# Kernel optimization log

Measured on AMD Instinct MI355X. Metric: run time of the kernel, lower is better.

The kernel has to match this reference:

```python
import jax, jax.numpy as jnp
import numpy as np

T, B, S, L = 256, 128, 256, 2
H, E, V = 512, 512, 32000


def setup_inputs() -> dict:
    key = jax.random.key(0)
    ks = jax.random.split(key, 17)
    n = lambda k, shape, s=0.05: jax.random.normal(k, shape, dtype=jnp.float32) * s
    tokens = jax.random.randint(ks[0], (T, B), 0, V)
    emb = n(ks[1], (V, E)).at[0].set(0.0)  # padding_idx=0 row zeroed
    return {
        "tokens": tokens,
        "h0": n(ks[2], (L, B, H)),
        "c0": n(ks[3], (L, B, H)),
        "context": n(ks[4], (S, B, H)),
        "init_output": n(ks[5], (B, H)),
        "emb": emb,
        "W_ih0": n(ks[6], (4 * H, E + H)),
        "b_ih0": n(ks[7], (4 * H,)),
        "W_hh0": n(ks[8], (4 * H, H)),
        "b_hh0": n(ks[9], (4 * H,)),
        "W_ih1": n(ks[10], (4 * H, H)),
        "b_ih1": n(ks[11], (4 * H,)),
        "W_hh1": n(ks[12], (4 * H, H)),
        "b_hh1": n(ks[13], (4 * H,)),
        "W_in": n(ks[14], (H, H)),
        "W_out": n(ks[15], (H, 2 * H)),
    }


def _lstm_cell(x, h, c, Wi, bi, Wh, bh):
    # torch LSTMCell: gates ordered i, f, g, o
    g = x @ Wi.T + bi + h @ Wh.T + bh
    i, f, gg, o = jnp.split(g, 4, axis=-1)
    c2 = jax.nn.sigmoid(f) * c + jax.nn.sigmoid(i) * jnp.tanh(gg)
    h2 = jax.nn.sigmoid(o) * jnp.tanh(c2)
    return h2, c2


def reference(tokens, h0, c0, context, init_output, emb,
              W_ih0, b_ih0, W_hh0, b_hh0, W_ih1, b_ih1, W_hh1, b_hh1,
              W_in, W_out):
    emb_seq = emb[tokens]                      # [T, B, E]
    ctx = jnp.transpose(context, (1, 0, 2))    # [B, S, H] (context.transpose(0,1))

    def step(carry, e_t):
        h, c, out = carry                      # h,c: [L,B,H]; out: [B,H]
        x = jnp.concatenate([e_t, out], axis=1)  # input feed
        h0_, c0_ = _lstm_cell(x, h[0], c[0], W_ih0, b_ih0, W_hh0, b_hh0)
        h1_, c1_ = _lstm_cell(h0_, h[1], c[1], W_ih1, b_ih1, W_hh1, b_hh1)
        rnn_out = h1_                          # dropout is identity at p=0 / eval
        # GlobalAttention (Luong general): score = ctx @ (W_in h)
        q = rnn_out @ W_in.T                   # [B, H]
        scores = jnp.einsum('bsh,bh->bs', ctx, q)
        a = jax.nn.softmax(scores, axis=-1)    # [B, S]
        wc = jnp.einsum('bs,bsh->bh', a, ctx)  # weighted context
        attn_out = jnp.tanh(jnp.concatenate([wc, rnn_out], axis=1) @ W_out.T)
        new_h = jnp.stack([h0_, h1_])
        new_c = jnp.stack([c0_, c1_])
        return (new_h, new_c, attn_out), (attn_out, a)

    (hF, cF, _), (outputs, attns) = jax.lax.scan(step, (h0, c0, init_output), emb_seq)
    return outputs, hF, cF, attns[-1]
```

## Files before the change

kernel.cpp:

```cpp
#include <hip/hip_runtime.h>
#include <hip/hip_bf16.h>
#include <math.h>

#define TT 256
#define BB 128
#define SS 256
#define HH 512
#define EE 512
#define NBLK 128
#define NTHR 512
#define BH (BB * HH)

typedef __attribute__((ext_vector_type(4))) float f32x4;
typedef __attribute__((ext_vector_type(2))) float f32x2;
typedef __attribute__((ext_vector_type(8))) short s16x8;
typedef unsigned long long u64;

__device__ __forceinline__ float b2f(short v) {
    union { unsigned u; float f; } c;
    c.u = ((unsigned)(unsigned short)v) << 16;
    return c.f;
}
__device__ __forceinline__ short f2b(float f) {
    union { float f; unsigned u; } c; c.f = f;
    unsigned u = c.u;
    unsigned r = (u + 0x7fffu + ((u >> 16) & 1u)) >> 16;
    return (short)r;
}
__device__ __forceinline__ float sigm(float x) { return 1.f / (1.f + __expf(-x)); }

__device__ __forceinline__ unsigned short f2fp8x2(float x, float y) {
    return (unsigned short)(__builtin_amdgcn_cvt_pk_fp8_f32(x, y, 0, false) & 0xffff);
}
__device__ __forceinline__ void f8x8(u64 q, float* o) {
    unsigned w0 = (unsigned)q, w1 = (unsigned)(q >> 32);
    f32x2 a = __builtin_amdgcn_cvt_pk_f32_fp8(w0, false);
    f32x2 b = __builtin_amdgcn_cvt_pk_f32_fp8(w0, true);
    f32x2 c = __builtin_amdgcn_cvt_pk_f32_fp8(w1, false);
    f32x2 d = __builtin_amdgcn_cvt_pk_f32_fp8(w1, true);
    o[0] = a[0]; o[1] = a[1]; o[2] = b[0]; o[3] = b[1];
    o[4] = c[0]; o[5] = c[1]; o[6] = d[0]; o[7] = d[1];
}

__device__ __forceinline__ u64 aldq(const void* p) {
    return __hip_atomic_load((const u64*)p, __ATOMIC_RELAXED, __HIP_MEMORY_SCOPE_AGENT);
}
__device__ __forceinline__ void ast2(short* p, short v) {
    __hip_atomic_store(p, v, __ATOMIC_RELAXED, __HIP_MEMORY_SCOPE_AGENT);
}
__device__ __forceinline__ s16x8 ald16(const void* p) {
    s16x8 r;
    asm volatile("global_load_dwordx4 %0, %1, off sc0 sc1" : "=v"(r) : "v"(p) : "memory");
    return r;
}

__device__ __forceinline__ void lbar() {
    asm volatile("s_waitcnt lgkmcnt(0)" ::: "memory");
    __builtin_amdgcn_s_barrier();
}


__global__ void k_pack2(const float* __restrict__ Wa, int ka, const float* __restrict__ Wb, int kb,
                        short* __restrict__ dst, int n) {
    const int K = ka + kb;
    for (int i = blockIdx.x * blockDim.x + threadIdx.x; i < n; i += gridDim.x * blockDim.x) {
        int g = i / K, k = i - g * K;
        float v = (k < ka) ? Wa[(size_t)g * ka + k] : Wb[(size_t)g * kb + (k - ka)];
        dst[i] = f2b(v);
    }
}

__global__ void k_bias(const float* __restrict__ a, const float* __restrict__ b, float* __restrict__ o,
                       const float* __restrict__ a2, const float* __restrict__ b2, float* __restrict__ o2) {
    int i = blockIdx.x * blockDim.x + threadIdx.x;
    if (i < 2048) { o[i] = a[i] + b[i]; o2[i] = a2[i] + b2[i]; }
}

__global__ void k_emb(const int* __restrict__ tok, const float* __restrict__ emb, short* __restrict__ Ebf) {
    const int n = TT * BB * EE;
    for (int i = blockIdx.x * blockDim.x + threadIdx.x; i < n; i += gridDim.x * blockDim.x) {
        int tb = i >> 9, k = i & 511;
        int t = tok[tb];
        Ebf[i] = f2b(emb[(size_t)t * EE + k]);
    }
}

__global__ void k_packwr(const float* __restrict__ Wout, unsigned* __restrict__ WRP) {
    int i = blockIdx.x * blockDim.x + threadIdx.x;
    if (i < 256 * 512) {
        int m = i >> 9, j = i & 511;
        unsigned lo = (unsigned)(unsigned short)f2b(Wout[(size_t)j * 1024 + 512 + 2 * m]);
        unsigned hi = (unsigned)(unsigned short)f2b(Wout[(size_t)j * 1024 + 512 + 2 * m + 1]);
        WRP[i] = lo | (hi << 16);
    }
}

__global__ __launch_bounds__(512) void k_cvt8(const float* __restrict__ ctx, const short* __restrict__ Wb,
                                              int wstride, unsigned char* __restrict__ out8) {
    const int tid = threadIdx.x, w = tid >> 6, l = tid & 63;
    const int m0 = blockIdx.y * 128, n0 = blockIdx.x * 64;
    const int kc8 = (l >> 4) * 8;
    const int m = m0 + w * 16 + (l & 15);
    const int b = m >> 8, s = m & 255;
    const float* arow = ctx + ((size_t)s * BB + b) * HH + kc8;
    f32x4 acc[4];
    const f32x4 zero = {0.f, 0.f, 0.f, 0.f};
#pragma unroll
    for (int j = 0; j < 4; ++j) acc[j] = zero;
#pragma unroll
    for (int kc = 0; kc < 16; ++kc) {
        const int k0 = kc * 32;
        float4 x0 = *reinterpret_cast<const float4*>(arow + k0);
        float4 x1 = *reinterpret_cast<const float4*>(arow + k0 + 4);
        s16x8 afr;
        afr[0] = f2b(x0.x); afr[1] = f2b(x0.y); afr[2] = f2b(x0.z); afr[3] = f2b(x0.w);
        afr[4] = f2b(x1.x); afr[5] = f2b(x1.y); afr[6] = f2b(x1.z); afr[7] = f2b(x1.w);
#pragma unroll
        for (int j = 0; j < 4; ++j) {
            s16x8 bfr = *reinterpret_cast<const s16x8*>(Wb + (size_t)(n0 + j * 16 + (l & 15)) * wstride + k0 + kc8);
            acc[j] = __builtin_amdgcn_mfma_f32_16x16x32_bf16(afr, bfr, acc[j], 0, 0, 0);
        }
    }
#pragma unroll
    for (int j = 0; j < 4; ++j)
#pragma unroll
        for (int r = 0; r < 4; ++r)
            out8[(size_t)(m0 + w * 16 + (l >> 4) * 4 + r) * HH + (n0 + j * 16 + (l & 15))] =
                (unsigned char)(__builtin_amdgcn_cvt_pk_fp8_f32(acc[j][r], 0.f, 0, false) & 0xff);
}

__global__ void k_state(const float* __restrict__ h0in, const float* __restrict__ iout,
                        short* __restrict__ h0x, short* __restrict__ h1x, short* __restrict__ outx) {
    int i = blockIdx.x * blockDim.x + threadIdx.x;
    if (i < BH) {
        h0x[i] = f2b(h0in[i]);
        h1x[i] = f2b(h0in[BH + i]);
        outx[i] = f2b(iout[i]);
    }
}


struct P {
    const short* Ebf;
    const float* c0in;
    const unsigned char* ctxW8;
    const unsigned char* ctxO8;
    const unsigned* WRP;
    const short* W0cat;
    const short* W1cat;
    const float* bias0;
    const float* bias1;
    short* h0x;
    short* h1x;
    short* outx;
    float* dout;
    unsigned* flags;
};

#define MFMA16(a, b, c) __builtin_amdgcn_mfma_f32_16x16x32_bf16((a), (b), (c), 0, 0, 0)

__device__ __forceinline__ s16x8 ldsfrag(const short* base, int stride, int row, int col8) {
    return *reinterpret_cast<const s16x8*>(base + row * stride + ((col8 ^ (row & 7)) << 3));
}

__device__ __forceinline__ void issue8(const short* __restrict__ src, int tid, int khalf, s16x8* q) {
#pragma unroll
    for (int c = 0; c < 8; ++c) {
        const int chunk = c * 512 + tid;
        const int row = chunk >> 5, col8 = chunk & 31;
        q[c] = ald16(src + row * HH + khalf * 256 + col8 * 8);
    }
}
template <int N>
__device__ __forceinline__ void write8n(short* __restrict__ stg, int tid, const s16x8* q) {
    asm volatile("s_waitcnt vmcnt(%0)" ::"i"(N) : "memory");
#pragma unroll
    for (int c = 0; c < 8; ++c) {
        const int chunk = c * 512 + tid;
        const int row = chunk >> 5, col8 = chunk & 31;
        *reinterpret_cast<s16x8*>(stg + row * 256 + ((col8 ^ (row & 7)) << 3)) = q[c];
    }
}

__device__ __forceinline__ f32x4 seg8(const short* stgp, const short* Ws, int wstride, int wbase,
                                      int mrow, int wrow, int kq, f32x4 acc) {
#pragma unroll
    for (int seg = 0; seg < 8; ++seg)
        acc = MFMA16(ldsfrag(stgp, 256, mrow, seg * 4 + kq),
                     ldsfrag(Ws, wstride, wrow, wbase + seg * 4 + kq), acc);
    return acc;
}

__device__ __forceinline__ void gbar(unsigned* flags, unsigned target) {
    asm volatile("s_waitcnt vmcnt(0)" ::: "memory");
    __syncthreads();
    if (threadIdx.x == 0)
        __hip_atomic_store(&flags[blockIdx.x], target, __ATOMIC_RELAXED, __HIP_MEMORY_SCOPE_AGENT);
    if (threadIdx.x < NBLK) {
        while (__hip_atomic_load(&flags[threadIdx.x], __ATOMIC_RELAXED, __HIP_MEMORY_SCOPE_AGENT) < target)
            __builtin_amdgcn_s_sleep(1);
    }
    __syncthreads();
}

__global__ void __launch_bounds__(NTHR, 1) coop_k(P p) {
    extern __shared__ __align__(16) char smem[];
    short* W0s = (short*)smem;
    short* W1s = W0s + 16 * 1536;
    short* stg = W1s + 16 * 1024;
    float* smallf = (float*)(stg + 128 * 256);
    float* bias0s = smallf;
    float* bias1s = smallf + 16;
    float* red = smallf + 32;
    float* scv = smallf + 48;
    float* aU = smallf + 304;
    float* h1f = smallf + 560;

    const int tid = threadIdx.x;
    const int blk = blockIdx.x;
    const int l = tid & 63;
    const int w = tid >> 6;
    const int lrow = l & 15;
    const int mrow = w * 16 + lrow;
    const int kq = l >> 4;
    const size_t OFF_HF = (size_t)TT * BH;
    const size_t OFF_CF = OFF_HF + 2 * (size_t)BH;
    const size_t OFF_AT = OFF_CF + 2 * (size_t)BH;
    const f32x4 fz = {0.f, 0.f, 0.f, 0.f};

    for (int idx = tid; idx < 16 * 192; idx += NTHR) {
        int row = idx / 192, col8 = idx % 192;
        int g = (row & 3) * 512 + blk * 4 + (row >> 2);
        *reinterpret_cast<s16x8*>(W0s + row * 1536 + ((col8 ^ (row & 7)) << 3)) =
            *reinterpret_cast<const s16x8*>(p.W0cat + (size_t)g * 1536 + col8 * 8);
    }
    for (int idx = tid; idx < 16 * 128; idx += NTHR) {
        int row = idx / 128, col8 = idx % 128;
        int g = (row & 3) * 512 + blk * 4 + (row >> 2);
        *reinterpret_cast<s16x8*>(W1s + row * 1024 + ((col8 ^ (row & 7)) << 3)) =
            *reinterpret_cast<const s16x8*>(p.W1cat + (size_t)g * 1024 + col8 * 8);
    }
    if (tid < 16) {
        int g = (tid & 3) * 512 + blk * 4 + (tid >> 2);
        bias0s[tid] = p.bias0[g];
        bias1s[tid] = p.bias1[g];
    }
    __syncthreads();

    const int bA = tid >> 2;
    const int jA = blk * 4 + (tid & 3);
    float c0reg = p.c0in[bA * HH + jA];
    float c1reg = p.c0in[BH + bA * HH + jA];
    unsigned ep = 0;
    s16x8 qa[8], qb[8], qc[8], qd[8];

    for (int t = 0; t < TT; ++t) {
        const size_t pB = (size_t)(t & 1) * BH;
        const size_t pN = (size_t)((t & 1) ^ 1) * BH;

        {
            issue8(p.outx + pB, tid, 0, qa);
            issue8(p.outx + pB, tid, 1, qb);
            f32x4 aE = fz, aO = fz, aH = fz;
            {
                const short* erow = p.Ebf + ((size_t)t * BB + mrow) * EE + kq * 8;
#pragma unroll
                for (int seg = 0; seg < 16; ++seg) {
                    s16x8 afr = *reinterpret_cast<const s16x8*>(erow + seg * 32);
                    aE = MFMA16(afr, ldsfrag(W0s, 1536, lrow, seg * 4 + kq), aE);
                }
            }
            write8n<8>(stg, tid, qa);
            issue8(p.h0x + pB, tid, 0, qc);
            lbar();
            aO = seg8(stg, W0s, 1536, 64, mrow, lrow, kq, aO);
            lbar();
            write8n<8>(stg, tid, qb);
            issue8(p.h0x + pB, tid, 1, qd);
            lbar();
            aO = seg8(stg, W0s, 1536, 96, mrow, lrow, kq, aO);
            lbar();
            write8n<8>(stg, tid, qc);
            lbar();
            aH = seg8(stg, W0s, 1536, 128, mrow, lrow, kq, aH);
            lbar();
            write8n<0>(stg, tid, qd);
            lbar();
            aH = seg8(stg, W0s, 1536, 160, mrow, lrow, kq, aH);

            f32x4 acc = aE + aO + aH;
            lbar();
            float* scr = (float*)stg + w * 272;
#pragma unroll
            for (int r = 0; r < 4; ++r) scr[lrow * 17 + kq * 4 + r] = acc[r];
            const int bloc = l >> 2;
            const int n0 = (l & 3) * 4;
            float gi = scr[(n0 + 0) * 17 + bloc] + bias0s[n0 + 0];
            float gf = scr[(n0 + 1) * 17 + bloc] + bias0s[n0 + 1];
            float gg = scr[(n0 + 2) * 17 + bloc] + bias0s[n0 + 2];
            float go = scr[(n0 + 3) * 17 + bloc] + bias0s[n0 + 3];
            float cn = sigm(gf) * c0reg + sigm(gi) * tanhf(gg);
            float hn = sigm(go) * tanhf(cn);
            c0reg = cn;
            ast2(&p.h0x[pN + bA * HH + jA], f2b(hn));
            if (t == TT - 1) {
                p.dout[OFF_HF + bA * HH + jA] = hn;
                p.dout[OFF_CF + bA * HH + jA] = cn;
            }
        }
        gbar(p.flags, ++ep);

        {
            issue8(p.h0x + pN, tid, 0, qa);
            issue8(p.h0x + pN, tid, 1, qb);
            f32x4 b0 = fz, b1 = fz;
            write8n<8>(stg, tid, qa);
            issue8(p.h1x + pB, tid, 0, qc);
            lbar();
            b0 = seg8(stg, W1s, 1024, 0, mrow, lrow, kq, b0);
            lbar();
            write8n<8>(stg, tid, qb);
            issue8(p.h1x + pB, tid, 1, qd);
            lbar();
            b0 = seg8(stg, W1s, 1024, 32, mrow, lrow, kq, b0);
            lbar();
            write8n<8>(stg, tid, qc);
            lbar();
            b1 = seg8(stg, W1s, 1024, 64, mrow, lrow, kq, b1);
            lbar();
            write8n<0>(stg, tid, qd);
            lbar();
            b1 = seg8(stg, W1s, 1024, 96, mrow, lrow, kq, b1);

            f32x4 acc = b0 + b1;
            lbar();
            float* scr = (float*)stg + w * 272;
#pragma unroll
            for (int r = 0; r < 4; ++r) scr[lrow * 17 + kq * 4 + r] = acc[r];
            const int bloc = l >> 2;
            const int n0 = (l & 3) * 4;
            float gi = scr[(n0 + 0) * 17 + bloc] + bias1s[n0 + 0];
            float gf = scr[(n0 + 1) * 17 + bloc] + bias1s[n0 + 1];
            float gg = scr[(n0 + 2) * 17 + bloc] + bias1s[n0 + 2];
            float go = scr[(n0 + 3) * 17 + bloc] + bias1s[n0 + 3];
            float cn = sigm(gf) * c1reg + sigm(gi) * tanhf(gg);
            float hn = sigm(go) * tanhf(cn);
            c1reg = cn;
            ast2(&p.h1x[pN + bA * HH + jA], f2b(hn));
            if (t == TT - 1) {
                p.dout[OFF_HF + BH + bA * HH + jA] = hn;
                p.dout[OFF_CF + BH + bA * HH + jA] = cn;
            }
        }
        gbar(p.flags, ++ep);

        {
            float* pF = (float*)stg;
            if (tid < 128) {
                union { u64 v; short s[4]; } c;
                c.v = aldq(p.h1x + pN + blk * HH + tid * 4);
#pragma unroll
                for (int j = 0; j < 4; ++j) h1f[tid * 4 + j] = b2f(c.s[j]);
            }
            lbar();
            float hreg[8];
#pragma unroll
            for (int j = 0; j < 8; ++j) hreg[j] = h1f[l * 8 + j];
            const unsigned char* cwb = p.ctxW8 + (size_t)blk * SS * HH;
#pragma unroll 4
            for (int it = 0; it < 32; ++it) {
                const int s = it * 8 + w;
                u64 q = *reinterpret_cast<const u64*>(cwb + (size_t)s * HH + l * 8);
                float o[8];
                f8x8(q, o);
                float pd = 0.f;
#pragma unroll
                for (int j = 0; j < 8; ++j) pd += o[j] * hreg[j];
#pragma unroll
                for (int off = 32; off; off >>= 1) pd += __shfl_xor(pd, off);
                if (l == 0) scv[s] = pd;
            }
            lbar();
            float sc = -1e30f, e = 0.f;
            if (tid < 256) sc = scv[tid];
            float mx = sc;
#pragma unroll
            for (int off = 32; off; off >>= 1) mx = fmaxf(mx, __shfl_xor(mx, off));
            if (l == 0 && tid < 256) red[w] = mx;
            lbar();
            const float M = fmaxf(fmaxf(red[0], red[1]), fmaxf(red[2], red[3]));
            if (tid < 256) { e = __expf(sc - M); aU[tid] = e; }
            float se = e;
#pragma unroll
            for (int off = 32; off; off >>= 1) se += __shfl_xor(se, off);
            if (l == 0 && tid < 256) red[8 + w] = se;
            lbar();
            const float inv = 1.f / (red[8] + red[9] + red[10] + red[11]);
            if (t == TT - 1 && tid < 256) p.dout[OFF_AT + blk * SS + tid] = aU[tid] * inv;
            const unsigned char* cob = p.ctxO8 + (size_t)blk * SS * HH;
            float wa[8];
#pragma unroll
            for (int j = 0; j < 8; ++j) wa[j] = 0.f;
#pragma unroll 4
            for (int it = 0; it < 32; ++it) {
                const int s = it * 8 + w;
                const float av = aU[s];
                u64 q = *reinterpret_cast<const u64*>(cob + (size_t)s * HH + l * 8);
                float o[8];
                f8x8(q, o);
#pragma unroll
                for (int j = 0; j < 8; ++j) wa[j] += av * o[j];
            }
            {
                float4* dst = reinterpret_cast<float4*>(pF + w * 512 + l * 8);
                float4 v0 = {wa[0], wa[1], wa[2], wa[3]};
                float4 v1 = {wa[4], wa[5], wa[6], wa[7]};
                dst[0] = v0;
                dst[1] = v1;
            }
            lbar();
            {
                float opv = 0.f;
#pragma unroll
                for (int ww = 0; ww < 8; ++ww) opv += pF[ww * 512 + tid];
                opv *= inv;
                const unsigned* wp = p.WRP + tid;
                float g = 0.f;
#pragma unroll 8
                for (int m = 0; m < 256; ++m) {
                    unsigned wv = wp[(size_t)m * 512];
                    g += b2f((short)(wv & 0xffff)) * h1f[2 * m] + b2f((short)(wv >> 16)) * h1f[2 * m + 1];
                }
                float tv = tanhf(opv + g);
                __builtin_nontemporal_store(tv, &p.dout[(size_t)t * BH + blk * HH + tid]);
                ast2(&p.outx[pN + blk * HH + tid], f2b(tv));
            }
        }
        gbar(p.flags, ++ep);
    }
}


extern "C" void kernel_launch(void* const* d_in, const int* in_sizes, int n_in,
                              void* d_out, int out_size, void* d_ws, size_t ws_size,
                              hipStream_t stream) {
    const int* tokens = (const int*)d_in[0];
    const float* h0in = (const float*)d_in[1];
    const float* c0in = (const float*)d_in[2];
    const float* ctx = (const float*)d_in[3];
    const float* iout = (const float*)d_in[4];
    const float* emb = (const float*)d_in[5];
    const float* Wih0 = (const float*)d_in[6];
    const float* bih0 = (const float*)d_in[7];
    const float* Whh0 = (const float*)d_in[8];
    const float* bhh0 = (const float*)d_in[9];
    const float* Wih1 = (const float*)d_in[10];
    const float* bih1 = (const float*)d_in[11];
    const float* Whh1 = (const float*)d_in[12];
    const float* bhh1 = (const float*)d_in[13];
    const float* Win = (const float*)d_in[14];
    const float* Wout = (const float*)d_in[15];
    float* dout = (float*)d_out;

    char* pw = (char*)d_ws;
    auto take = [&](size_t bytes) { char* r = pw; pw += (bytes + 255) & ~(size_t)255; return r; };
    short* W0cat = (short*)take((size_t)2048 * 1536 * 2);
    short* W1cat = (short*)take((size_t)2048 * 1024 * 2);
    short* Winb  = (short*)take((size_t)512 * 512 * 2);
    short* Woutb = (short*)take((size_t)512 * 1024 * 2);
    unsigned* WRP = (unsigned*)take((size_t)256 * 512 * 4);
    float* bias0 = (float*)take(2048 * 4);
    float* bias1 = (float*)take(2048 * 4);
    short* Ebf   = (short*)take((size_t)TT * BB * EE * 2);
    unsigned char* ctxW8 = (unsigned char*)take((size_t)BB * SS * HH);
    unsigned char* ctxO8 = (unsigned char*)take((size_t)BB * SS * HH);
    short* h0x   = (short*)take((size_t)2 * BH * 2);
    short* h1x   = (short*)take((size_t)2 * BH * 2);
    short* outx  = (short*)take((size_t)2 * BH * 2);
    unsigned* flags = (unsigned*)take(NBLK * 4);

    k_pack2<<<2048, 256, 0, stream>>>(Wih0, 1024, Whh0, 512, W0cat, 2048 * 1536);
    k_pack2<<<2048, 256, 0, stream>>>(Wih1, 512, Whh1, 512, W1cat, 2048 * 1024);
    k_pack2<<<1024, 256, 0, stream>>>(Win, 512, Win, 0, Winb, 512 * 512);
    k_pack2<<<1024, 256, 0, stream>>>(Wout, 1024, Wout, 0, Woutb, 512 * 1024);
    k_packwr<<<512, 256, 0, stream>>>(Wout, WRP);
    k_bias<<<8, 256, 0, stream>>>(bih0, bhh0, bias0, bih1, bhh1, bias1);
    k_emb<<<4096, 256, 0, stream>>>(tokens, emb, Ebf);
    k_state<<<256, 256, 0, stream>>>(h0in, iout, h0x, h1x, outx);
    k_cvt8<<<dim3(8, 256), 512, 0, stream>>>(ctx, Winb, 512, ctxW8);
    k_cvt8<<<dim3(8, 256), 512, 0, stream>>>(ctx, Woutb, 1024, ctxO8);
    (void)hipMemsetAsync(flags, 0, NBLK * 4, stream);

    const unsigned smem_bytes = (16 * 1536 + 16 * 1024 + 128 * 256) * 2 + (16 + 16 + 16 + 256 + 256 + 512) * 4;
    (void)hipFuncSetAttribute((const void*)coop_k, hipFuncAttributeMaxDynamicSharedMemorySize, (int)smem_bytes);

    P prm;
    prm.Ebf = Ebf; prm.c0in = c0in;
    prm.ctxW8 = ctxW8; prm.ctxO8 = ctxO8; prm.WRP = WRP;
    prm.W0cat = W0cat; prm.W1cat = W1cat;
    prm.bias0 = bias0; prm.bias1 = bias1;
    prm.h0x = h0x; prm.h1x = h1x; prm.outx = outx;
    prm.dout = dout; prm.flags = flags;
    void* args[] = {&prm};
    (void)hipLaunchCooperativeKernel((void*)coop_k, dim3(NBLK), dim3(NTHR), args, smem_bytes, stream);
}
```

Before: 14.80 ms.

## Use FP8 and BF16 MFMA for attention scores, context mix and output projection

The per-step attention work moves from scalar FP32 dot products to matrix instructions. Scores against the precomputed ctx·W_in are now done with fp8 MFMA, and the weighted context uses a transposed fp8 ctx·W_out buffer with fp8 MFMA. The h1 part of the output projection uses bf16 MFMA on Woutb instead of a scalar loop over the packed WRP. Both h1 and the attention weights are now quantized to fp8, which adds precision risk. Only lane 0 of each 16-column MFMA result is used, so most of the MFMA throughput goes to unused rows.

```diff
diff --git a/kernel.cpp b/kernel.cpp
--- a/kernel.cpp
+++ b/kernel.cpp
@@ -12,7 +12,6 @@
 #define BH (BB * HH)
 
 typedef __attribute__((ext_vector_type(4))) float f32x4;
-typedef __attribute__((ext_vector_type(2))) float f32x2;
 typedef __attribute__((ext_vector_type(8))) short s16x8;
 typedef unsigned long long u64;
 
@@ -28,19 +27,6 @@
     return (short)r;
 }
 __device__ __forceinline__ float sigm(float x) { return 1.f / (1.f + __expf(-x)); }
-
-__device__ __forceinline__ unsigned short f2fp8x2(float x, float y) {
-    return (unsigned short)(__builtin_amdgcn_cvt_pk_fp8_f32(x, y, 0, false) & 0xffff);
-}
-__device__ __forceinline__ void f8x8(u64 q, float* o) {
-    unsigned w0 = (unsigned)q, w1 = (unsigned)(q >> 32);
-    f32x2 a = __builtin_amdgcn_cvt_pk_f32_fp8(w0, false);
-    f32x2 b = __builtin_amdgcn_cvt_pk_f32_fp8(w0, true);
-    f32x2 c = __builtin_amdgcn_cvt_pk_f32_fp8(w1, false);
-    f32x2 d = __builtin_amdgcn_cvt_pk_f32_fp8(w1, true);
-    o[0] = a[0]; o[1] = a[1]; o[2] = b[0]; o[3] = b[1];
-    o[4] = c[0]; o[5] = c[1]; o[6] = d[0]; o[7] = d[1];
-}
 
 __device__ __forceinline__ u64 aldq(const void* p) {
     return __hip_atomic_load((const u64*)p, __ATOMIC_RELAXED, __HIP_MEMORY_SCOPE_AGENT);
@@ -85,18 +71,8 @@
     }
 }
 
-__global__ void k_packwr(const float* __restrict__ Wout, unsigned* __restrict__ WRP) {
-    int i = blockIdx.x * blockDim.x + threadIdx.x;
-    if (i < 256 * 512) {
-        int m = i >> 9, j = i & 511;
-        unsigned lo = (unsigned)(unsigned short)f2b(Wout[(size_t)j * 1024 + 512 + 2 * m]);
-        unsigned hi = (unsigned)(unsigned short)f2b(Wout[(size_t)j * 1024 + 512 + 2 * m + 1]);
-        WRP[i] = lo | (hi << 16);
-    }
-}
-
 __global__ __launch_bounds__(512) void k_cvt8(const float* __restrict__ ctx, const short* __restrict__ Wb,
-                                              int wstride, unsigned char* __restrict__ out8) {
+                                              int wstride, int transpose, unsigned char* __restrict__ out8) {
     const int tid = threadIdx.x, w = tid >> 6, l = tid & 63;
     const int m0 = blockIdx.y * 128, n0 = blockIdx.x * 64;
     const int kc8 = (l >> 4) * 8;
@@ -124,9 +100,17 @@
 #pragma unroll
     for (int j = 0; j < 4; ++j)
 #pragma unroll
-        for (int r = 0; r < 4; ++r)
-            out8[(size_t)(m0 + w * 16 + (l >> 4) * 4 + r) * HH + (n0 + j * 16 + (l & 15))] =
-                (unsigned char)(__builtin_amdgcn_cvt_pk_fp8_f32(acc[j][r], 0.f, 0, false) & 0xff);
+        for (int r = 0; r < 4; ++r) {
+            const int mm = m0 + w * 16 + (l >> 4) * 4 + r;
+            const int nn = n0 + j * 16 + (l & 15);
+            unsigned char v8 = (unsigned char)(__builtin_amdgcn_cvt_pk_fp8_f32(acc[j][r], 0.f, 0, false) & 0xff);
+            if (transpose) {
+                const int bb = mm >> 8, ss = mm & 255;
+                out8[((size_t)bb * HH + nn) * SS + ss] = v8;
+            } else {
+                out8[(size_t)mm * HH + nn] = v8;
+            }
+        }
 }
 
 __global__ void k_state(const float* __restrict__ h0in, const float* __restrict__ iout,
@@ -144,8 +128,8 @@
     const short* Ebf;
     const float* c0in;
     const unsigned char* ctxW8;
-    const unsigned char* ctxO8;
-    const unsigned* WRP;
+    const unsigned char* ctxO8T;
+    const short* Woutb;
     const short* W0cat;
     const short* W1cat;
     const float* bias0;
@@ -158,6 +142,7 @@
 };
 
 #define MFMA16(a, b, c) __builtin_amdgcn_mfma_f32_16x16x32_bf16((a), (b), (c), 0, 0, 0)
+#define MFMA8(a, b, c) __builtin_amdgcn_mfma_f32_16x16x32_fp8_fp8((a), (b), (c), 0, 0, 0)
 
 __device__ __forceinline__ s16x8 ldsfrag(const short* base, int stride, int row, int col8) {
     return *reinterpret_cast<const s16x8*>(base + row * stride + ((col8 ^ (row & 7)) << 3));
@@ -214,7 +199,9 @@
     float* red = smallf + 32;
     float* scv = smallf + 48;
     float* aU = smallf + 304;
-    float* h1f = smallf + 560;
+    short* h1b = (short*)(smallf + 560);
+    unsigned* h18u = (unsigned*)(smallf + 816);
+    unsigned* a32 = (unsigned*)(smallf + 944);
 
     const int tid = threadIdx.x;
     const int blk = blockIdx.x;
@@ -355,30 +342,34 @@
         gbar(p.flags, ++ep);
 
         {
-            float* pF = (float*)stg;
+            float* pFh = (float*)stg;
             if (tid < 128) {
                 union { u64 v; short s[4]; } c;
                 c.v = aldq(p.h1x + pN + blk * HH + tid * 4);
 #pragma unroll
-                for (int j = 0; j < 4; ++j) h1f[tid * 4 + j] = b2f(c.s[j]);
-            }
-            lbar();
-            float hreg[8];
-#pragma unroll
-            for (int j = 0; j < 8; ++j) hreg[j] = h1f[l * 8 + j];
-            const unsigned char* cwb = p.ctxW8 + (size_t)blk * SS * HH;
-#pragma unroll 4
-            for (int it = 0; it < 32; ++it) {
-                const int s = it * 8 + w;
-                u64 q = *reinterpret_cast<const u64*>(cwb + (size_t)s * HH + l * 8);
-                float o[8];
-                f8x8(q, o);
-                float pd = 0.f;
-#pragma unroll
-                for (int j = 0; j < 8; ++j) pd += o[j] * hreg[j];
-#pragma unroll
-                for (int off = 32; off; off >>= 1) pd += __shfl_xor(pd, off);
-                if (l == 0) scv[s] = pd;
+                for (int j = 0; j < 4; ++j) h1b[tid * 4 + j] = c.s[j];
+                float f0 = b2f(c.s[0]), f1 = b2f(c.s[1]), f2 = b2f(c.s[2]), f3 = b2f(c.s[3]);
+                unsigned lo = __builtin_amdgcn_cvt_pk_fp8_f32(f0, f1, 0, false) & 0xffffu;
+                unsigned hi = __builtin_amdgcn_cvt_pk_fp8_f32(f2, f3, 0, false) & 0xffffu;
+                h18u[tid] = lo | (hi << 16);
+            }
+            lbar();
+            {
+                const unsigned char* cwb = p.ctxW8 + (size_t)blk * SS * HH;
+                const u64* h18q = (const u64*)h18u;
+#pragma unroll
+                for (int i = 0; i < 2; ++i) {
+                    const int s0 = (w * 2 + i) * 16;
+                    f32x4 acc = fz;
+#pragma unroll
+                    for (int kc = 0; kc < 16; ++kc) {
+                        const int k0 = kc * 32;
+                        long long av = (long long)h18q[(k0 >> 3) + kq];
+                        long long bv = *reinterpret_cast<const long long*>(cwb + (size_t)(s0 + lrow) * HH + k0 + kq * 8);
+                        acc = MFMA8(av, bv, acc);
+                    }
+                    if (l < 16) scv[s0 + l] = acc[0];
+                }
             }
             lbar();
             float sc = -1e30f, e = 0.f;
@@ -397,43 +388,52 @@
             lbar();
             const float inv = 1.f / (red[8] + red[9] + red[10] + red[11]);
             if (t == TT - 1 && tid < 256) p.dout[OFF_AT + blk * SS + tid] = aU[tid] * inv;
-            const unsigned char* cob = p.ctxO8 + (size_t)blk * SS * HH;
-            float wa[8];
-#pragma unroll
-            for (int j = 0; j < 8; ++j) wa[j] = 0.f;
-#pragma unroll 4
-            for (int it = 0; it < 32; ++it) {
-                const int s = it * 8 + w;
-                const float av = aU[s];
-                u64 q = *reinterpret_cast<const u64*>(cob + (size_t)s * HH + l * 8);
-                float o[8];
-                f8x8(q, o);
-#pragma unroll
-                for (int j = 0; j < 8; ++j) wa[j] += av * o[j];
-            }
+            if (tid < 64) {
+                unsigned lo = __builtin_amdgcn_cvt_pk_fp8_f32(aU[tid * 4], aU[tid * 4 + 1], 0, false) & 0xffffu;
+                unsigned hi = __builtin_amdgcn_cvt_pk_fp8_f32(aU[tid * 4 + 2], aU[tid * 4 + 3], 0, false) & 0xffffu;
+                a32[tid] = lo | (hi << 16);
+            }
+            f32x4 gacc[4];
+#pragma unroll
+            for (int i = 0; i < 4; ++i) {
+                const int j0 = (w * 4 + i) * 16;
+                f32x4 acc = fz;
+#pragma unroll
+                for (int kc = 0; kc < 16; ++kc) {
+                    const int k0 = kc * 32;
+                    s16x8 av = *reinterpret_cast<const s16x8*>(h1b + k0 + kq * 8);
+                    s16x8 bv = *reinterpret_cast<const s16x8*>(p.Woutb + (size_t)(j0 + lrow) * 1024 + 512 + k0 + kq * 8);
+                    acc = MFMA16(av, bv, acc);
+                }
+                gacc[i] = acc;
+            }
+            lbar();
             {
-                float4* dst = reinterpret_cast<float4*>(pF + w * 512 + l * 8);
-                float4 v0 = {wa[0], wa[1], wa[2], wa[3]};
-                float4 v1 = {wa[4], wa[5], wa[6], wa[7]};
-                dst[0] = v0;
-                dst[1] = v1;
-            }
-            lbar();
-            {
-                float opv = 0.f;
-#pragma unroll
-                for (int ww = 0; ww < 8; ++ww) opv += pF[ww * 512 + tid];
-                opv *= inv;
-                const unsigned* wp = p.WRP + tid;
-                float g = 0.f;
-#pragma unroll 8
-                for (int m = 0; m < 256; ++m) {
-                    unsigned wv = wp[(size_t)m * 512];
-                    g += b2f((short)(wv & 0xffff)) * h1f[2 * m] + b2f((short)(wv >> 16)) * h1f[2 * m + 1];
+                const unsigned char* cob = p.ctxO8T + (size_t)blk * HH * SS;
+                const u64* a8q = (const u64*)a32;
+#pragma unroll
+                for (int i = 0; i < 4; ++i) {
+                    const int h0 = (w * 4 + i) * 16;
+                    f32x4 acc = fz;
+#pragma unroll
+                    for (int kc = 0; kc < 8; ++kc) {
+                        const int k0 = kc * 32;
+                        long long av = (long long)a8q[(k0 >> 3) + kq];
+                        long long bv = *reinterpret_cast<const long long*>(cob + (size_t)(h0 + lrow) * SS + k0 + kq * 8);
+                        acc = MFMA8(av, bv, acc);
+                    }
+                    if (l < 16) pFh[h0 + l] = acc[0];
                 }
-                float tv = tanhf(opv + g);
-                __builtin_nontemporal_store(tv, &p.dout[(size_t)t * BH + blk * HH + tid]);
-                ast2(&p.outx[pN + blk * HH + tid], f2b(tv));
+            }
+            lbar();
+#pragma unroll
+            for (int i = 0; i < 4; ++i) {
+                if (l < 16) {
+                    const int j = (w * 4 + i) * 16 + l;
+                    float tv = tanhf(pFh[j] * inv + gacc[i][0]);
+                    __builtin_nontemporal_store(tv, &p.dout[(size_t)t * BH + blk * HH + j]);
+                    ast2(&p.outx[pN + blk * HH + j], f2b(tv));
+                }
             }
         }
         gbar(p.flags, ++ep);
@@ -468,12 +468,11 @@
     short* W1cat = (short*)take((size_t)2048 * 1024 * 2);
     short* Winb  = (short*)take((size_t)512 * 512 * 2);
     short* Woutb = (short*)take((size_t)512 * 1024 * 2);
-    unsigned* WRP = (unsigned*)take((size_t)256 * 512 * 4);
     float* bias0 = (float*)take(2048 * 4);
     float* bias1 = (float*)take(2048 * 4);
     short* Ebf   = (short*)take((size_t)TT * BB * EE * 2);
     unsigned char* ctxW8 = (unsigned char*)take((size_t)BB * SS * HH);
-    unsigned char* ctxO8 = (unsigned char*)take((size_t)BB * SS * HH);
+    unsigned char* ctxO8T = (unsigned char*)take((size_t)BB * SS * HH);
     short* h0x   = (short*)take((size_t)2 * BH * 2);
     short* h1x   = (short*)take((size_t)2 * BH * 2);
     short* outx  = (short*)take((size_t)2 * BH * 2);
@@ -483,20 +482,19 @@
     k_pack2<<<2048, 256, 0, stream>>>(Wih1, 512, Whh1, 512, W1cat, 2048 * 1024);
     k_pack2<<<1024, 256, 0, stream>>>(Win, 512, Win, 0, Winb, 512 * 512);
     k_pack2<<<1024, 256, 0, stream>>>(Wout, 1024, Wout, 0, Woutb, 512 * 1024);
-    k_packwr<<<512, 256, 0, stream>>>(Wout, WRP);
     k_bias<<<8, 256, 0, stream>>>(bih0, bhh0, bias0, bih1, bhh1, bias1);
     k_emb<<<4096, 256, 0, stream>>>(tokens, emb, Ebf);
     k_state<<<256, 256, 0, stream>>>(h0in, iout, h0x, h1x, outx);
-    k_cvt8<<<dim3(8, 256), 512, 0, stream>>>(ctx, Winb, 512, ctxW8);
-    k_cvt8<<<dim3(8, 256), 512, 0, stream>>>(ctx, Woutb, 1024, ctxO8);
+    k_cvt8<<<dim3(8, 256), 512, 0, stream>>>(ctx, Winb, 512, 0, ctxW8);
+    k_cvt8<<<dim3(8, 256), 512, 0, stream>>>(ctx, Woutb, 1024, 1, ctxO8T);
     (void)hipMemsetAsync(flags, 0, NBLK * 4, stream);
 
-    const unsigned smem_bytes = (16 * 1536 + 16 * 1024 + 128 * 256) * 2 + (16 + 16 + 16 + 256 + 256 + 512) * 4;
+    const unsigned smem_bytes = (16 * 1536 + 16 * 1024 + 128 * 256) * 2 + 1008 * 4;
     (void)hipFuncSetAttribute((const void*)coop_k, hipFuncAttributeMaxDynamicSharedMemorySize, (int)smem_bytes);
 
     P prm;
     prm.Ebf = Ebf; prm.c0in = c0in;
-    prm.ctxW8 = ctxW8; prm.ctxO8 = ctxO8; prm.WRP = WRP;
+    prm.ctxW8 = ctxW8; prm.ctxO8T = ctxO8T; prm.Woutb = Woutb;
     prm.W0cat = W0cat; prm.W1cat = W1cat;
     prm.bias0 = bias0; prm.bias1 = bias1;
     prm.h0x = h0x; prm.h1x = h1x; prm.outx = outx;
```

Measured after the change: 14.58 ms. About the same (-1.5%).
